# Optimization experiments

Hardware: AMD Instinct MI355X
Metric: run time of the kernel (lower is better)

Reference implementation:

```python
import jax, jax.numpy as jnp
from jax import lax
import numpy as np


def _conv(x, w):
    # x: [B,Cin,H,W], w: [Cout,Cin,kh,kw] -> [B,Cout,H,W], SAME padding
    return lax.conv_general_dilated(x, w, (1, 1), 'SAME')


def setup_inputs() -> dict:
    key = jax.random.key(0)
    ks = jax.random.split(key, 16)
    B, Hh, W = 8, 256, 256
    inputs = jax.random.normal(ks[0], (B, Hh, W), jnp.float32)
    H0 = jax.random.normal(ks[1], (B, Hh, W), jnp.float32)
    C0 = jax.random.normal(ks[2], (B, 2, Hh, W), jnp.float32)
    # learned scalars: c2 ~ U(0,1), sf ~ N(0, 0.01) shifted away from 0 (it is a divisor)
    c2 = jax.random.uniform(ks[3], (1,), jnp.float32, 0.0, 1.0)
    sf = 0.01 * jax.random.normal(ks[4], (1,), jnp.float32) + 0.02
    # RedNet (assumed small conv encoder-decoder): 1->32->64->32->1, 3x3 SAME, ReLU
    w1 = 0.1 * jax.random.normal(ks[5], (32, 1, 3, 3), jnp.float32)
    b1 = jnp.zeros((32,), jnp.float32)
    w2 = 0.1 * jax.random.normal(ks[6], (64, 32, 3, 3), jnp.float32)
    b2 = jnp.zeros((64,), jnp.float32)
    w3 = 0.1 * jax.random.normal(ks[7], (32, 64, 3, 3), jnp.float32)
    b3 = jnp.zeros((32,), jnp.float32)
    w4 = 0.1 * jax.random.normal(ks[8], (1, 32, 3, 3), jnp.float32)
    b4 = jnp.zeros((1,), jnp.float32)
    return dict(inputs=inputs, H0=H0, C0=C0, c2=c2, sf=sf,
                w1=w1, b1=b1, w2=w2, b2=b2, w3=w3, b3=b3, w4=w4, b4=b4)


def reference(inputs, H0, C0, c2, sf, w1, b1, w2, b2, w3, b3, w4, b4):
    # Fixed 5-point Laplacian stencil (non-trainable in the original module)
    lap_k = jnp.array([[0., 1., 0.], [1., -4., 1.], [0., 1., 0.]],
                      dtype=inputs.dtype)[None, None]  # [1,1,3,3]

    # torch chain: C' = permute/matmul(Wcc^T)/permute + wcu*U
    #   reduces exactly to: C'[:,0] = inputs, C'[:,1] = C_old[:,0]
    C_new = jnp.stack([inputs, C0[:, 0]], axis=1)  # [B,2,H,W]

    V = inputs - H0  # [B,H,W]

    # H = whc . C' = 2*C'[:,0] - C'[:,1] = 2*inputs - C_old[:,0]
    lap = _conv(inputs[:, None], lap_k)[:, 0]  # [B,H,W]
    H = 2.0 * inputs - C0[:, 0] + c2 * lap

    # RedNet on scaled residual V
    h = (V / sf)[:, None]  # [B,1,H,W]
    h = jax.nn.relu(_conv(h, w1) + b1[None, :, None, None])
    h = jax.nn.relu(_conv(h, w2) + b2[None, :, None, None])
    h = jax.nn.relu(_conv(h, w3) + b3[None, :, None, None])
    V_hat = (_conv(h, w4) + b4[None, :, None, None])[:, 0] * sf  # [B,H,W]

    outputs = H + V_hat
    return (outputs, H, C_new, V, V_hat)
```

## Files before the change

kernel.cpp:

```cpp
#include <hip/hip_runtime.h>

#define PLANE 65536
#define WIDTH 256
#define PADW 258
#define PADPLANE 66564

typedef __bf16 v8bf __attribute__((ext_vector_type(8)));
typedef float  v4f  __attribute__((ext_vector_type(4)));

typedef const __attribute__((address_space(1))) unsigned int* gas_ptr;
typedef __attribute__((address_space(3))) unsigned int* las_ptr;

__device__ __forceinline__ void gl_lds(const void* g, void* l) {
  __builtin_amdgcn_global_load_lds((gas_ptr)g, (las_ptr)l, 16, 0, 0);
}

__device__ __forceinline__ int swz(int c) {
  return (c & ~7) | ((c & 7) ^ ((c >> 3) & 7));
}

__device__ __forceinline__ unsigned int pack2(float a, float b) {
  __bf16 ba = (__bf16)a, bb = (__bf16)b;
  unsigned short sa = __builtin_bit_cast(unsigned short, ba);
  unsigned short sb = __builtin_bit_cast(unsigned short, bb);
  return (unsigned int)sa | ((unsigned int)sb << 16);
}

__global__ __launch_bounds__(256) void prep_k(
    const float* __restrict__ inputs, const float* __restrict__ H0,
    const float* __restrict__ C0, const float* __restrict__ c2p,
    const float* __restrict__ sfp, float* __restrict__ dout,
    float* __restrict__ vs)
{
  int p = blockIdx.x * 256 + threadIdx.x;
  int b = p >> 16;
  int i = p & 65535;
  int y = i >> 8;
  int x = i & 255;
  float in   = inputs[p];
  float h0   = H0[p];
  float c0a  = C0[b * 131072 + i];
  float up    = (y > 0)   ? inputs[p - 256] : 0.f;
  float down  = (y < 255) ? inputs[p + 256] : 0.f;
  float left  = (x > 0)   ? inputs[p - 1]   : 0.f;
  float right = (x < 255) ? inputs[p + 1]   : 0.f;
  float lap = up + down + left + right - 4.f * in;
  float c2 = c2p[0];
  float sf = sfp[0];
  float Hv = 2.f * in - c0a + c2 * lap;
  float V  = in - h0;
  dout[524288 + p]  = Hv;
  dout[2097152 + p] = V;
  dout[1048576 + b * 131072 + i]         = in;
  dout[1048576 + b * 131072 + 65536 + i] = c0a;
  vs[p] = V / sf;
}

__global__ __launch_bounds__(256) void wtrans_k(
    const float* __restrict__ w1, const float* __restrict__ w2,
    const float* __restrict__ w3, const float* __restrict__ w4,
    float* __restrict__ w1t, __bf16* __restrict__ B2t,
    __bf16* __restrict__ B3t, float* __restrict__ w4t)
{
  int t = blockIdx.x * 256 + threadIdx.x;
  if (t < 288) {
    int tap = t >> 5, cout = t & 31;
    w1t[t] = w1[cout * 9 + tap];
  }
  int t2 = t - 288;
  if (t2 >= 0 && t2 < 18432) {
    int cout = t2 / 288, k = t2 % 288;
    int tap = k / 32, cin = k % 32;
    B2t[t2] = (__bf16)w2[cout * 288 + cin * 9 + tap];
  }
  int t3 = t - (288 + 18432);
  if (t3 >= 0 && t3 < 18432) {
    int cout = t3 / 576, k = t3 % 576;
    int tap = k / 64, cin = k % 64;
    B3t[t3] = (__bf16)w3[cout * 576 + cin * 9 + tap];
  }
  int t4 = t - (288 + 18432 + 18432);
  if (t4 >= 0 && t4 < 288) {
    int tap = t4 >> 5, cin = t4 & 31;
    w4t[t4] = w4[cin * 9 + tap];
  }
}

#define R1 (8 * 1028 * 16)
#define R2 (8 * 1028 * 32)
#define R3 (8 * 1028 * 16)
__global__ __launch_bounds__(256) void zero_k(
    __bf16* __restrict__ a1, __bf16* __restrict__ a2, __bf16* __restrict__ a3)
{
  int t = blockIdx.x * 256 + threadIdx.x;
  unsigned int* p; int C2, idx;
  if (t < R1)            { p = (unsigned int*)a1; C2 = 16; idx = t; }
  else if (t < R1 + R2)  { p = (unsigned int*)a2; C2 = 32; idx = t - R1; }
  else if (t < R1+R2+R3) { p = (unsigned int*)a3; C2 = 16; idx = t - R1 - R2; }
  else return;
  int ch = idx % C2;
  int pr = idx / C2;
  int b = pr / 1028, r = pr % 1028;
  int y, x;
  if      (r < 258) { y = 0;           x = r; }
  else if (r < 516) { y = 257;         x = r - 258; }
  else if (r < 772) { y = r - 516 + 1; x = 0; }
  else              { y = r - 772 + 1; x = 257; }
  p[((size_t)b * PADPLANE + y * PADW + x) * C2 + ch] = 0;
}

__global__ __launch_bounds__(256) void conv1_k(
    const float* __restrict__ vs, const float* __restrict__ w1t,
    const float* __restrict__ b1, __bf16* __restrict__ act1)
{
  int x = threadIdx.x, y = blockIdx.x, b = blockIdx.y;
  const float* ip = vs + ((size_t)b << 16) + y * WIDTH + x;
  float acc[32];
  #pragma unroll
  for (int i = 0; i < 32; i++) acc[i] = b1[i];
  #pragma unroll
  for (int tap = 0; tap < 9; tap++) {
    int dy = tap / 3 - 1, dx = tap % 3 - 1;
    int yy = y + dy, xx = x + dx;
    bool ok = (yy >= 0 && yy < 256 && xx >= 0 && xx < 256);
    float v = ok ? ip[dy * WIDTH + dx] : 0.f;
    const float* wp = w1t + tap * 32;
    #pragma unroll
    for (int i = 0; i < 32; i++) acc[i] = fmaf(wp[i], v, acc[i]);
  }
  unsigned int u[16];
  #pragma unroll
  for (int j = 0; j < 16; j++)
    u[j] = pack2(fmaxf(acc[2*j], 0.f), fmaxf(acc[2*j+1], 0.f));
  size_t pa = ((size_t)b * PADPLANE + (y+1) * PADW + (x+1)) * 32;
  uint4* op = reinterpret_cast<uint4*>(act1 + pa);
  #pragma unroll
  for (int j = 0; j < 4; j++)
    op[j] = make_uint4(u[4*j], u[4*j+1], u[4*j+2], u[4*j+3]);
}

template<int CIN, int COUT, int ROWS>
__global__ __launch_bounds__(256) void conv_lds_k(
    const __bf16* __restrict__ in, const __bf16* __restrict__ Bt,
    const float* __restrict__ bias, __bf16* __restrict__ out)
{
  constexpr int CP    = CIN / 8;
  constexpr int KB    = CIN / 32;
  constexpr int NT    = COUT / 32;
  constexpr int ROWCH = 130 * CP;
  constexpr int ROWB  = ROWCH * 16;
  constexpr int K9    = 9 * CIN;
  constexpr int PWCH  = ROWCH / 4;

  const int lane = threadIdx.x & 63, wave = threadIdx.x >> 6;
  const int l15 = lane & 15, q = lane >> 4;
  const int mw = wave >> 1, nw = wave & 1;
  const int y0 = blockIdx.x * ROWS, xt = blockIdx.y, b = blockIdx.z;
  __shared__ __align__(16) char smem[3 * ROWB];
  const __bf16* plane = in + (size_t)b * PADPLANE * CIN;

  auto stage = [&](int pr, char* lrow) {
    const char* g = (const char*)(plane + ((size_t)pr * PADW + xt * 128) * CIN);
    const int base = wave * PWCH;
    #pragma unroll
    for (int j = 0; j < PWCH / 64; j++) {
      int c = base + j * 64 + lane;
      gl_lds(g + (size_t)swz(c) * 16, lrow + (base + j * 64) * 16);
    }
    if (lane < (PWCH % 64)) {
      int c = base + (PWCH / 64) * 64 + lane;
      gl_lds(g + (size_t)swz(c) * 16, lrow + (base + (PWCH / 64) * 64) * 16);
    }
  };

  v8bf breg[9][KB * NT];
  #pragma unroll
  for (int tap = 0; tap < 9; tap++)
    #pragma unroll
    for (int kb = 0; kb < KB; kb++)
      #pragma unroll
      for (int nt = 0; nt < NT; nt++)
        breg[tap][kb * NT + nt] = *(const v8bf*)(Bt
            + (size_t)(nw * (COUT / 2) + nt * 16 + l15) * K9
            + tap * CIN + kb * 32 + q * 8);

  #pragma unroll
  for (int r = 0; r < 3; r++) stage(y0 + r, smem + r * ROWB);
  __syncthreads();

  for (int i = 0; i < ROWS; i++) {
    v4f acc[4][NT];
    #pragma unroll
    for (int nt = 0; nt < NT; nt++) {
      float bv = bias[nw * (COUT / 2) + nt * 16 + l15];
      #pragma unroll
      for (int mt = 0; mt < 4; mt++) acc[mt][nt] = (v4f){bv, bv, bv, bv};
    }
    #pragma unroll
    for (int tap = 0; tap < 9; tap++) {
      const int dy = tap / 3, dx = tap % 3;
      const char* srow = smem + ((i + dy) % 3) * ROWB;
      #pragma unroll
      for (int kb = 0; kb < KB; kb++) {
        v8bf af[4];
        #pragma unroll
        for (int mt = 0; mt < 4; mt++) {
          int p = mw * 64 + mt * 16 + l15 + dx;
          int G = p * CP + kb * 4 + q;
          af[mt] = *(const v8bf*)(srow + (size_t)swz(G) * 16);
        }
        #pragma unroll
        for (int mt = 0; mt < 4; mt++)
          #pragma unroll
          for (int nt = 0; nt < NT; nt++)
            acc[mt][nt] = __builtin_amdgcn_mfma_f32_16x16x32_bf16(
                af[mt], breg[tap][kb * NT + nt], acc[mt][nt], 0, 0, 0);
      }
    }
    {
      size_t rb = ((size_t)b * PADPLANE + (size_t)(y0 + i + 1) * PADW
                   + xt * 128 + 1) * COUT;
      #pragma unroll
      for (int mt = 0; mt < 4; mt++) {
        #pragma unroll
        for (int r = 0; r < 4; r++) {
          size_t pa = rb + (size_t)(mw * 64 + mt * 16 + q * 4 + r) * COUT;
          #pragma unroll
          for (int nt = 0; nt < NT; nt++)
            out[pa + nw * (COUT / 2) + nt * 16 + l15] =
                (__bf16)fmaxf(acc[mt][nt][r], 0.f);
        }
      }
    }
    __syncthreads();
    if (i + 3 < ROWS + 2)
      stage(y0 + i + 3, smem + (i % 3) * ROWB);
    __syncthreads();
  }
}

#define C4ROWS 4
__global__ __launch_bounds__(256) void conv4_k(
    const __bf16* __restrict__ act3, const float* __restrict__ w4t,
    const float* __restrict__ b4, const float* __restrict__ sfp,
    float* __restrict__ dout)
{
  const int x = threadIdx.x, y0 = blockIdx.x * C4ROWS, b = blockIdx.y;
  const float b4v = b4[0], sf = sfp[0];
  const uint4* base = (const uint4*)(act3 + (size_t)b * PADPLANE * 32);
  float accs[3] = {b4v, b4v, b4v};

  #pragma unroll
  for (int t = 0; t < C4ROWS + 2; t++) {
    const int pr = y0 + t;
    const uint4* rp = base + ((size_t)pr * PADW + x) * 4;
    uint4 L[12];
    #pragma unroll
    for (int j = 0; j < 12; j++) L[j] = rp[j];
    #pragma unroll
    for (int j = 0; j < 12; j++) {
      const int dx = j >> 2, c0 = (j & 3) * 8;
      unsigned int uu[4] = {L[j].x, L[j].y, L[j].z, L[j].w};
      float f[8];
      #pragma unroll
      for (int k = 0; k < 4; k++) {
        f[2*k]   = __builtin_bit_cast(float, uu[k] << 16);
        f[2*k+1] = __builtin_bit_cast(float, uu[k] & 0xFFFF0000u);
      }
      #pragma unroll
      for (int dyp = 0; dyp < 3; dyp++) {
        if (dyp <= t && t - dyp < C4ROWS) {
          const int slot = (t - dyp) % 3;
          const float* wp = w4t + (dyp * 3 + dx) * 32 + c0;
          #pragma unroll
          for (int k = 0; k < 8; k++)
            accs[slot] = fmaf(wp[k], f[k], accs[slot]);
        }
      }
    }
    if (t >= 2) {
      const int r = y0 + t - 2, slot = (t - 2) % 3;
      size_t p0 = ((size_t)b << 16) + (size_t)r * WIDTH + x;
      float vh = accs[slot] * sf;
      dout[p0]           = dout[524288 + p0] + vh;
      dout[2621440 + p0] = vh;
      accs[slot] = b4v;
    }
  }
}

extern "C" void kernel_launch(void* const* d_in, const int* in_sizes, int n_in,
                              void* d_out, int out_size, void* d_ws, size_t ws_size,
                              hipStream_t stream) {
  const float* inputs = (const float*)d_in[0];
  const float* H0     = (const float*)d_in[1];
  const float* C0     = (const float*)d_in[2];
  const float* c2     = (const float*)d_in[3];
  const float* sf     = (const float*)d_in[4];
  const float* w1     = (const float*)d_in[5];
  const float* b1     = (const float*)d_in[6];
  const float* w2     = (const float*)d_in[7];
  const float* b2     = (const float*)d_in[8];
  const float* w3     = (const float*)d_in[9];
  const float* b3     = (const float*)d_in[10];
  const float* w4     = (const float*)d_in[11];
  const float* b4     = (const float*)d_in[12];
  float* out = (float*)d_out;
  float* ws  = (float*)d_ws;

  float*  vs   = ws;
  float*  w1t  = ws + 524288;
  float*  w4t  = ws + 524576;
  __bf16* B2t  = (__bf16*)(ws + 524864);
  __bf16* B3t  = (__bf16*)(ws + 534080);
  __bf16* act1 = (__bf16*)(ws + 543296);
  __bf16* act2 = act1 + (size_t)8 * PADPLANE * 32;
  __bf16* act3 = act2 + (size_t)8 * PADPLANE * 64;

  prep_k<<<2048, 256, 0, stream>>>(inputs, H0, C0, c2, sf, out, vs);
  wtrans_k<<<147, 256, 0, stream>>>(w1, w2, w3, w4, w1t, B2t, B3t, w4t);
  zero_k<<<2056, 256, 0, stream>>>(act1, act2, act3);
  conv1_k<<<dim3(256, 8), 256, 0, stream>>>(vs, w1t, b1, act1);
  conv_lds_k<32, 64, 4><<<dim3(64, 2, 8), 256, 0, stream>>>(act1, B2t, b2, act2);
  conv_lds_k<64, 32, 4><<<dim3(64, 2, 8), 256, 0, stream>>>(act2, B3t, b3, act3);
  conv4_k<<<dim3(64, 8), 256, 0, stream>>>(act3, w4t, b4, sf, out);
}
```

Measured before the change: 192.1 us.

## Specialize conv2/conv3 kernels with full-N waves and two-row reuse in conv3

Replaces the generic templated MFMA conv kernel with two specialized versions. Each wave now covers all output channels for 32 pixels instead of splitting N across waves. conv3 computes two output rows per step from a 4-row LDS ring, so each A fragment loaded from LDS feeds both rows. Both kernels also process 8 rows per block with launch bounds asking for 2 blocks per CU. The aim is fewer LDS reads and less halo restaging per output, at the cost of more registers, larger LDS use and half as many blocks.

```diff
diff --git a/kernel.cpp b/kernel.cpp
--- a/kernel.cpp
+++ b/kernel.cpp
@@ -139,102 +139,196 @@
     op[j] = make_uint4(u[4*j], u[4*j+1], u[4*j+2], u[4*j+3]);
 }
 
-template<int CIN, int COUT, int ROWS>
-__global__ __launch_bounds__(256) void conv_lds_k(
+#define C2ROWB 8320
+template<int ROWS>
+__global__ __launch_bounds__(256, 2) void conv2_k(
     const __bf16* __restrict__ in, const __bf16* __restrict__ Bt,
     const float* __restrict__ bias, __bf16* __restrict__ out)
 {
-  constexpr int CP    = CIN / 8;
-  constexpr int KB    = CIN / 32;
-  constexpr int NT    = COUT / 32;
-  constexpr int ROWCH = 130 * CP;
-  constexpr int ROWB  = ROWCH * 16;
-  constexpr int K9    = 9 * CIN;
-  constexpr int PWCH  = ROWCH / 4;
-
   const int lane = threadIdx.x & 63, wave = threadIdx.x >> 6;
   const int l15 = lane & 15, q = lane >> 4;
-  const int mw = wave >> 1, nw = wave & 1;
   const int y0 = blockIdx.x * ROWS, xt = blockIdx.y, b = blockIdx.z;
-  __shared__ __align__(16) char smem[3 * ROWB];
-  const __bf16* plane = in + (size_t)b * PADPLANE * CIN;
+  const int x0 = xt * 128;
+  __shared__ __align__(16) char smem[3 * C2ROWB];
+  const __bf16* plane = in + (size_t)b * PADPLANE * 32;
 
   auto stage = [&](int pr, char* lrow) {
-    const char* g = (const char*)(plane + ((size_t)pr * PADW + xt * 128) * CIN);
-    const int base = wave * PWCH;
-    #pragma unroll
-    for (int j = 0; j < PWCH / 64; j++) {
+    const char* g = (const char*)(plane + ((size_t)pr * PADW + x0) * 32);
+    const int base = wave * 130;
+    #pragma unroll
+    for (int j = 0; j < 2; j++) {
       int c = base + j * 64 + lane;
       gl_lds(g + (size_t)swz(c) * 16, lrow + (base + j * 64) * 16);
     }
-    if (lane < (PWCH % 64)) {
-      int c = base + (PWCH / 64) * 64 + lane;
-      gl_lds(g + (size_t)swz(c) * 16, lrow + (base + (PWCH / 64) * 64) * 16);
+    if (lane < 2) {
+      int c = base + 128 + lane;
+      gl_lds(g + (size_t)swz(c) * 16, lrow + (base + 128) * 16);
     }
   };
 
-  v8bf breg[9][KB * NT];
+  v8bf breg[9][4];
   #pragma unroll
   for (int tap = 0; tap < 9; tap++)
     #pragma unroll
-    for (int kb = 0; kb < KB; kb++)
-      #pragma unroll
-      for (int nt = 0; nt < NT; nt++)
-        breg[tap][kb * NT + nt] = *(const v8bf*)(Bt
-            + (size_t)(nw * (COUT / 2) + nt * 16 + l15) * K9
-            + tap * CIN + kb * 32 + q * 8);
-
-  #pragma unroll
-  for (int r = 0; r < 3; r++) stage(y0 + r, smem + r * ROWB);
+    for (int nt = 0; nt < 4; nt++)
+      breg[tap][nt] = *(const v8bf*)(Bt + (size_t)(nt * 16 + l15) * 288
+                                        + tap * 32 + q * 8);
+  float bv[4];
+  #pragma unroll
+  for (int nt = 0; nt < 4; nt++) bv[nt] = bias[nt * 16 + l15];
+
+  #pragma unroll
+  for (int r = 0; r < 3; r++) stage(y0 + r, smem + r * C2ROWB);
   __syncthreads();
 
   for (int i = 0; i < ROWS; i++) {
-    v4f acc[4][NT];
-    #pragma unroll
-    for (int nt = 0; nt < NT; nt++) {
-      float bv = bias[nw * (COUT / 2) + nt * 16 + l15];
-      #pragma unroll
-      for (int mt = 0; mt < 4; mt++) acc[mt][nt] = (v4f){bv, bv, bv, bv};
-    }
+    v4f acc[2][4];
+    #pragma unroll
+    for (int mt = 0; mt < 2; mt++)
+      #pragma unroll
+      for (int nt = 0; nt < 4; nt++)
+        acc[mt][nt] = (v4f){bv[nt], bv[nt], bv[nt], bv[nt]};
+
     #pragma unroll
     for (int tap = 0; tap < 9; tap++) {
       const int dy = tap / 3, dx = tap % 3;
-      const char* srow = smem + ((i + dy) % 3) * ROWB;
-      #pragma unroll
-      for (int kb = 0; kb < KB; kb++) {
-        v8bf af[4];
+      const char* srow = smem + ((i + dy) % 3) * C2ROWB;
+      v8bf af[2];
+      #pragma unroll
+      for (int mt = 0; mt < 2; mt++) {
+        int P = wave * 32 + mt * 16 + l15 + dx;
+        af[mt] = *(const v8bf*)(srow + (size_t)swz(P * 4 + q) * 16);
+      }
+      #pragma unroll
+      for (int mt = 0; mt < 2; mt++)
         #pragma unroll
-        for (int mt = 0; mt < 4; mt++) {
-          int p = mw * 64 + mt * 16 + l15 + dx;
-          int G = p * CP + kb * 4 + q;
-          af[mt] = *(const v8bf*)(srow + (size_t)swz(G) * 16);
-        }
-        #pragma unroll
-        for (int mt = 0; mt < 4; mt++)
-          #pragma unroll
-          for (int nt = 0; nt < NT; nt++)
-            acc[mt][nt] = __builtin_amdgcn_mfma_f32_16x16x32_bf16(
-                af[mt], breg[tap][kb * NT + nt], acc[mt][nt], 0, 0, 0);
-      }
+        for (int nt = 0; nt < 4; nt++)
+          acc[mt][nt] = __builtin_amdgcn_mfma_f32_16x16x32_bf16(
+              af[mt], breg[tap][nt], acc[mt][nt], 0, 0, 0);
     }
     {
       size_t rb = ((size_t)b * PADPLANE + (size_t)(y0 + i + 1) * PADW
-                   + xt * 128 + 1) * COUT;
-      #pragma unroll
-      for (int mt = 0; mt < 4; mt++) {
+                   + x0 + 1) * 64;
+      #pragma unroll
+      for (int mt = 0; mt < 2; mt++) {
         #pragma unroll
         for (int r = 0; r < 4; r++) {
-          size_t pa = rb + (size_t)(mw * 64 + mt * 16 + q * 4 + r) * COUT;
+          size_t pa = rb + (size_t)(wave * 32 + mt * 16 + q * 4 + r) * 64;
           #pragma unroll
-          for (int nt = 0; nt < NT; nt++)
-            out[pa + nw * (COUT / 2) + nt * 16 + l15] =
-                (__bf16)fmaxf(acc[mt][nt][r], 0.f);
+          for (int nt = 0; nt < 4; nt++)
+            out[pa + nt * 16 + l15] = (__bf16)fmaxf(acc[mt][nt][r], 0.f);
         }
       }
     }
     __syncthreads();
     if (i + 3 < ROWS + 2)
-      stage(y0 + i + 3, smem + (i % 3) * ROWB);
+      stage(y0 + i + 3, smem + (i % 3) * C2ROWB);
+    __syncthreads();
+  }
+}
+
+#define C3ROWB 16640
+template<int ROWS>
+__global__ __launch_bounds__(256, 2) void conv3_k(
+    const __bf16* __restrict__ in, const __bf16* __restrict__ Bt,
+    const float* __restrict__ bias, __bf16* __restrict__ out)
+{
+  const int lane = threadIdx.x & 63, wave = threadIdx.x >> 6;
+  const int l15 = lane & 15, q = lane >> 4;
+  const int y0 = blockIdx.x * ROWS, xt = blockIdx.y, b = blockIdx.z;
+  const int x0 = xt * 128;
+  __shared__ __align__(16) char smem[4 * C3ROWB];
+  const __bf16* plane = in + (size_t)b * PADPLANE * 64;
+
+  auto stage = [&](int pr, char* lrow) {
+    const char* g = (const char*)(plane + ((size_t)pr * PADW + x0) * 64);
+    const int base = wave * 260;
+    #pragma unroll
+    for (int j = 0; j < 4; j++) {
+      int c = base + j * 64 + lane;
+      gl_lds(g + (size_t)swz(c) * 16, lrow + (base + j * 64) * 16);
+    }
+    if (lane < 4) {
+      int c = base + 256 + lane;
+      gl_lds(g + (size_t)swz(c) * 16, lrow + (base + 256) * 16);
+    }
+  };
+
+  v8bf breg[9][2][2];
+  #pragma unroll
+  for (int tap = 0; tap < 9; tap++)
+    #pragma unroll
+    for (int kb = 0; kb < 2; kb++)
+      #pragma unroll
+      for (int nt = 0; nt < 2; nt++)
+        breg[tap][kb][nt] = *(const v8bf*)(Bt + (size_t)(nt * 16 + l15) * 576
+                                              + tap * 64 + kb * 32 + q * 8);
+  float bv[2] = {bias[l15], bias[16 + l15]};
+
+  #pragma unroll
+  for (int r = 0; r < 4; r++) stage(y0 + r, smem + r * C3ROWB);
+  __syncthreads();
+
+  for (int ps = 0; ps < ROWS / 2; ps++) {
+    v4f acc[2][2][2];
+    #pragma unroll
+    for (int rr = 0; rr < 2; rr++)
+      #pragma unroll
+      for (int mt = 0; mt < 2; mt++)
+        #pragma unroll
+        for (int nt = 0; nt < 2; nt++)
+          acc[rr][mt][nt] = (v4f){bv[nt], bv[nt], bv[nt], bv[nt]};
+
+    #pragma unroll
+    for (int t = 0; t < 4; t++) {
+      const char* srow = smem + ((2 * ps + t) & 3) * C3ROWB;
+      #pragma unroll
+      for (int dx = 0; dx < 3; dx++) {
+        #pragma unroll
+        for (int kb = 0; kb < 2; kb++) {
+          v8bf af[2];
+          #pragma unroll
+          for (int mt = 0; mt < 2; mt++) {
+            int P = wave * 32 + mt * 16 + l15 + dx;
+            af[mt] = *(const v8bf*)(srow + (size_t)swz(P * 8 + kb * 4 + q) * 16);
+          }
+          #pragma unroll
+          for (int mt = 0; mt < 2; mt++)
+            #pragma unroll
+            for (int nt = 0; nt < 2; nt++) {
+              if (t <= 2)
+                acc[0][mt][nt] = __builtin_amdgcn_mfma_f32_16x16x32_bf16(
+                    af[mt], breg[t * 3 + dx][kb][nt], acc[0][mt][nt], 0, 0, 0);
+              if (t >= 1)
+                acc[1][mt][nt] = __builtin_amdgcn_mfma_f32_16x16x32_bf16(
+                    af[mt], breg[(t - 1) * 3 + dx][kb][nt], acc[1][mt][nt],
+                    0, 0, 0);
+            }
+        }
+      }
+    }
+    {
+      #pragma unroll
+      for (int rr = 0; rr < 2; rr++) {
+        size_t rb = ((size_t)b * PADPLANE
+                     + (size_t)(y0 + 2 * ps + rr + 1) * PADW + x0 + 1) * 32;
+        #pragma unroll
+        for (int mt = 0; mt < 2; mt++) {
+          #pragma unroll
+          for (int r = 0; r < 4; r++) {
+            size_t pa = rb + (size_t)(wave * 32 + mt * 16 + q * 4 + r) * 32;
+            #pragma unroll
+            for (int nt = 0; nt < 2; nt++)
+              out[pa + nt * 16 + l15] = (__bf16)fmaxf(acc[rr][mt][nt][r], 0.f);
+          }
+        }
+      }
+    }
+    __syncthreads();
+    if (ps + 1 < ROWS / 2) {
+      stage(y0 + 2 * ps + 4, smem + ((2 * ps) & 3) * C3ROWB);
+      stage(y0 + 2 * ps + 5, smem + ((2 * ps + 1) & 3) * C3ROWB);
+    }
     __syncthreads();
   }
 }
@@ -321,7 +415,7 @@
   wtrans_k<<<147, 256, 0, stream>>>(w1, w2, w3, w4, w1t, B2t, B3t, w4t);
   zero_k<<<2056, 256, 0, stream>>>(act1, act2, act3);
   conv1_k<<<dim3(256, 8), 256, 0, stream>>>(vs, w1t, b1, act1);
-  conv_lds_k<32, 64, 4><<<dim3(64, 2, 8), 256, 0, stream>>>(act1, B2t, b2, act2);
-  conv_lds_k<64, 32, 4><<<dim3(64, 2, 8), 256, 0, stream>>>(act2, B3t, b3, act3);
+  conv2_k<8><<<dim3(32, 2, 8), 256, 0, stream>>>(act1, B2t, b2, act2);
+  conv3_k<8><<<dim3(32, 2, 8), 256, 0, stream>>>(act2, B3t, b3, act3);
   conv4_k<<<dim3(64, 8), 256, 0, stream>>>(act3, w4t, b4, sf, out);
 }
```

Result: faster. 187.8 us (-2.3%).

## Fuse conv2 and conv3 into one kernel keeping act2 rows in LDS

Applied to the files above, without the earlier changes.

Replaces the two separate conv_lds_k launches with a single conv23_k that computes conv2 rows into a rolling 3-row LDS buffer and immediately consumes them for conv3, so the 64-channel act2 tensor is never written to or read from global memory. The act2 padding zeroing is dropped from zero_k accordingly. Tiles become 32-row by 64-column slabs, with halo recomputation at the column edges and a grid of only 256 blocks with launch_bounds(256,1). This cuts global traffic at the cost of lower parallelism, halo recompute, and more syncs per row.

```diff
diff --git a/kernel.cpp b/kernel.cpp
--- a/kernel.cpp
+++ b/kernel.cpp
@@ -87,26 +87,24 @@
 }
 
 #define R1 (8 * 1028 * 16)
-#define R2 (8 * 1028 * 32)
 #define R3 (8 * 1028 * 16)
 __global__ __launch_bounds__(256) void zero_k(
-    __bf16* __restrict__ a1, __bf16* __restrict__ a2, __bf16* __restrict__ a3)
+    __bf16* __restrict__ a1, __bf16* __restrict__ a3)
 {
   int t = blockIdx.x * 256 + threadIdx.x;
-  unsigned int* p; int C2, idx;
-  if (t < R1)            { p = (unsigned int*)a1; C2 = 16; idx = t; }
-  else if (t < R1 + R2)  { p = (unsigned int*)a2; C2 = 32; idx = t - R1; }
-  else if (t < R1+R2+R3) { p = (unsigned int*)a3; C2 = 16; idx = t - R1 - R2; }
+  unsigned int* p; int idx;
+  if (t < R1)            { p = (unsigned int*)a1; idx = t; }
+  else if (t < R1 + R3)  { p = (unsigned int*)a3; idx = t - R1; }
   else return;
-  int ch = idx % C2;
-  int pr = idx / C2;
+  int ch = idx & 15;
+  int pr = idx >> 4;
   int b = pr / 1028, r = pr % 1028;
   int y, x;
   if      (r < 258) { y = 0;           x = r; }
   else if (r < 516) { y = 257;         x = r - 258; }
   else if (r < 772) { y = r - 516 + 1; x = 0; }
   else              { y = r - 772 + 1; x = 257; }
-  p[((size_t)b * PADPLANE + y * PADW + x) * C2 + ch] = 0;
+  p[((size_t)b * PADPLANE + y * PADW + x) * 16 + ch] = 0;
 }
 
 __global__ __launch_bounds__(256) void conv1_k(
@@ -139,102 +137,167 @@
     op[j] = make_uint4(u[4*j], u[4*j+1], u[4*j+2], u[4*j+3]);
 }
 
-template<int CIN, int COUT, int ROWS>
-__global__ __launch_bounds__(256) void conv_lds_k(
-    const __bf16* __restrict__ in, const __bf16* __restrict__ Bt,
-    const float* __restrict__ bias, __bf16* __restrict__ out)
-{
-  constexpr int CP    = CIN / 8;
-  constexpr int KB    = CIN / 32;
-  constexpr int NT    = COUT / 32;
-  constexpr int ROWCH = 130 * CP;
-  constexpr int ROWB  = ROWCH * 16;
-  constexpr int K9    = 9 * CIN;
-  constexpr int PWCH  = ROWCH / 4;
+#define A1SLOT 5376
+#define A2SLOT 10496
+#define SLAB23 32
+
+__global__ __launch_bounds__(256, 1) void conv23_k(
+    const __bf16* __restrict__ act1, const __bf16* __restrict__ B2t,
+    const __bf16* __restrict__ B3t, const float* __restrict__ b2,
+    const float* __restrict__ b3, __bf16* __restrict__ act3)
+{
+  __shared__ __align__(16) char sm1[4 * A1SLOT];
+  __shared__ __align__(16) char sm2[3 * A2SLOT];
 
   const int lane = threadIdx.x & 63, wave = threadIdx.x >> 6;
   const int l15 = lane & 15, q = lane >> 4;
-  const int mw = wave >> 1, nw = wave & 1;
-  const int y0 = blockIdx.x * ROWS, xt = blockIdx.y, b = blockIdx.z;
-  __shared__ __align__(16) char smem[3 * ROWB];
-  const __bf16* plane = in + (size_t)b * PADPLANE * CIN;
-
-  auto stage = [&](int pr, char* lrow) {
-    const char* g = (const char*)(plane + ((size_t)pr * PADW + xt * 128) * CIN);
-    const int base = wave * PWCH;
-    #pragma unroll
-    for (int j = 0; j < PWCH / 64; j++) {
-      int c = base + j * 64 + lane;
-      gl_lds(g + (size_t)swz(c) * 16, lrow + (base + j * 64) * 16);
-    }
-    if (lane < (PWCH % 64)) {
-      int c = base + (PWCH / 64) * 64 + lane;
-      gl_lds(g + (size_t)swz(c) * 16, lrow + (base + (PWCH / 64) * 64) * 16);
+  const int y0 = blockIdx.x * SLAB23;
+  const int x0 = blockIdx.y * 64;
+  const int b  = blockIdx.z;
+  const int s2 = (x0 == 0) ? 1 : 0;
+  const int z2 = (x0 == 0) ? 0 : ((x0 == 192) ? 65 : -1);
+  const int gcol0 = x0 - 1;
+  const int nmt = (wave == 0) ? 2 : 1;
+
+  const char* plane1 = (const char*)(act1 + (size_t)b * PADPLANE * 32);
+
+  v8bf b2r[9][4];
+  float bv2[4];
+  #pragma unroll
+  for (int tap = 0; tap < 9; tap++)
+    #pragma unroll
+    for (int nt = 0; nt < 4; nt++)
+      b2r[tap][nt] = *(const v8bf*)(B2t + (size_t)(nt * 16 + l15) * 288
+                                        + tap * 32 + q * 8);
+  #pragma unroll
+  for (int nt = 0; nt < 4; nt++) bv2[nt] = b2[nt * 16 + l15];
+
+  v8bf b3r[9][2][2];
+  float bv3[2];
+  #pragma unroll
+  for (int tap = 0; tap < 9; tap++)
+    #pragma unroll
+    for (int kb = 0; kb < 2; kb++)
+      #pragma unroll
+      for (int nt = 0; nt < 2; nt++)
+        b3r[tap][kb][nt] = *(const v8bf*)(B3t + (size_t)(nt * 16 + l15) * 576
+                                              + tap * 64 + kb * 32 + q * 8);
+  bv3[0] = b3[l15]; bv3[1] = b3[16 + l15];
+
+  auto stage1 = [&](int rr) {
+    if (rr < -1 || rr > 256) return;
+    char* lrow = sm1 + (size_t)((rr + 4) & 3) * A1SLOT;
+    const char* g = plane1 + (long)((rr + 1) * PADW + gcol0) * 64;
+    const int base = wave * 68;
+    {
+      int c = base + lane;
+      gl_lds(g + (long)swz(c) * 16, lrow + (size_t)base * 16);
+    }
+    if (lane < 4) {
+      int c = base + 64 + lane;
+      gl_lds(g + (long)swz(c) * 16, lrow + (size_t)(base + 64) * 16);
     }
   };
 
-  v8bf breg[9][KB * NT];
-  #pragma unroll
-  for (int tap = 0; tap < 9; tap++)
-    #pragma unroll
-    for (int kb = 0; kb < KB; kb++)
-      #pragma unroll
-      for (int nt = 0; nt < NT; nt++)
-        breg[tap][kb * NT + nt] = *(const v8bf*)(Bt
-            + (size_t)(nw * (COUT / 2) + nt * 16 + l15) * K9
-            + tap * CIN + kb * 32 + q * 8);
-
-  #pragma unroll
-  for (int r = 0; r < 3; r++) stage(y0 + r, smem + r * ROWB);
-  __syncthreads();
-
-  for (int i = 0; i < ROWS; i++) {
-    v4f acc[4][NT];
-    #pragma unroll
-    for (int nt = 0; nt < NT; nt++) {
-      float bv = bias[nw * (COUT / 2) + nt * 16 + l15];
-      #pragma unroll
-      for (int mt = 0; mt < 4; mt++) acc[mt][nt] = (v4f){bv, bv, bv, bv};
-    }
+  auto conv2row = [&](int n2) {
+    char* wr = sm2 + (size_t)(((n2 % 3) + 3) % 3) * A2SLOT;
+    if (n2 < 0 || n2 > 255) {
+      for (int c = threadIdx.x; c < 528; c += 256)
+        *(uint4*)(wr + (size_t)c * 16) = make_uint4(0, 0, 0, 0);
+      return;
+    }
+    const char* a1p[3];
+    #pragma unroll
+    for (int dy = 0; dy < 3; dy++)
+      a1p[dy] = sm1 + (size_t)((n2 - 1 + dy + 4) & 3) * A1SLOT;
+    v4f acc[2][4];
+    #pragma unroll
+    for (int mi = 0; mi < 2; mi++)
+      #pragma unroll
+      for (int nt = 0; nt < 4; nt++)
+        acc[mi][nt] = (v4f){bv2[nt], bv2[nt], bv2[nt], bv2[nt]};
     #pragma unroll
     for (int tap = 0; tap < 9; tap++) {
       const int dy = tap / 3, dx = tap % 3;
-      const char* srow = smem + ((i + dy) % 3) * ROWB;
-      #pragma unroll
-      for (int kb = 0; kb < KB; kb++) {
-        v8bf af[4];
+      v8bf af[2];
+      #pragma unroll
+      for (int mi = 0; mi < 2; mi++) if (mi < nmt) {
+        int tile = (mi == 0) ? wave : 4;
+        int w = s2 + tile * 16 + l15 + dx;
+        af[mi] = *(const v8bf*)(a1p[dy] + (size_t)swz(w * 4 + q) * 16);
+      }
+      #pragma unroll
+      for (int mi = 0; mi < 2; mi++) if (mi < nmt)
         #pragma unroll
-        for (int mt = 0; mt < 4; mt++) {
-          int p = mw * 64 + mt * 16 + l15 + dx;
-          int G = p * CP + kb * 4 + q;
-          af[mt] = *(const v8bf*)(srow + (size_t)swz(G) * 16);
-        }
+        for (int nt = 0; nt < 4; nt++)
+          acc[mi][nt] = __builtin_amdgcn_mfma_f32_16x16x32_bf16(
+              af[mi], b2r[tap][nt], acc[mi][nt], 0, 0, 0);
+    }
+    #pragma unroll
+    for (int mi = 0; mi < 2; mi++) if (mi < nmt) {
+      int tile = (mi == 0) ? wave : 4;
+      #pragma unroll
+      for (int r = 0; r < 4; r++) {
+        int p = s2 + tile * 16 + q * 4 + r;
         #pragma unroll
-        for (int mt = 0; mt < 4; mt++)
-          #pragma unroll
-          for (int nt = 0; nt < NT; nt++)
-            acc[mt][nt] = __builtin_amdgcn_mfma_f32_16x16x32_bf16(
-                af[mt], breg[tap][kb * NT + nt], acc[mt][nt], 0, 0, 0);
-      }
-    }
-    {
-      size_t rb = ((size_t)b * PADPLANE + (size_t)(y0 + i + 1) * PADW
-                   + xt * 128 + 1) * COUT;
-      #pragma unroll
-      for (int mt = 0; mt < 4; mt++) {
-        #pragma unroll
-        for (int r = 0; r < 4; r++) {
-          size_t pa = rb + (size_t)(mw * 64 + mt * 16 + q * 4 + r) * COUT;
-          #pragma unroll
-          for (int nt = 0; nt < NT; nt++)
-            out[pa + nw * (COUT / 2) + nt * 16 + l15] =
-                (__bf16)fmaxf(acc[mt][nt][r], 0.f);
+        for (int nt = 0; nt < 4; nt++) {
+          int c = p * 8 + nt * 2 + (l15 >> 3);
+          *(__bf16*)(wr + (size_t)swz(c) * 16 + (l15 & 7) * 2) =
+              (__bf16)fmaxf(acc[mi][nt][r], 0.f);
         }
       }
     }
+    if (z2 >= 0 && threadIdx.x < 8)
+      *(uint4*)(wr + (size_t)swz(z2 * 8 + (int)threadIdx.x) * 16) =
+          make_uint4(0, 0, 0, 0);
+  };
+
+  auto conv3row = [&](int r3) {
+    v4f acc[2];
+    #pragma unroll
+    for (int nt = 0; nt < 2; nt++)
+      acc[nt] = (v4f){bv3[nt], bv3[nt], bv3[nt], bv3[nt]};
+    #pragma unroll
+    for (int t = 0; t < 3; t++) {
+      const char* ar = sm2 + (size_t)((r3 - 1 + t + 3) % 3) * A2SLOT;
+      #pragma unroll
+      for (int dx = 0; dx < 3; dx++)
+        #pragma unroll
+        for (int kb = 0; kb < 2; kb++) {
+          int j = wave * 16 + l15;
+          v8bf af = *(const v8bf*)(ar
+              + (size_t)swz((j + dx) * 8 + kb * 4 + q) * 16);
+          #pragma unroll
+          for (int nt = 0; nt < 2; nt++)
+            acc[nt] = __builtin_amdgcn_mfma_f32_16x16x32_bf16(
+                af, b3r[t * 3 + dx][kb][nt], acc[nt], 0, 0, 0);
+        }
+    }
+    size_t rb = ((size_t)b * PADPLANE + (size_t)(r3 + 1) * PADW + x0 + 1) * 32;
+    #pragma unroll
+    for (int r = 0; r < 4; r++) {
+      int j = wave * 16 + q * 4 + r;
+      #pragma unroll
+      for (int nt = 0; nt < 2; nt++)
+        act3[rb + (size_t)j * 32 + nt * 16 + l15] =
+            (__bf16)fmaxf(acc[nt][r], 0.f);
+    }
+  };
+
+  stage1(y0 - 2); stage1(y0 - 1); stage1(y0); stage1(y0 + 1);
+  __syncthreads();
+  conv2row(y0 - 1);
+  __syncthreads();
+  stage1(y0 + 2);
+  conv2row(y0);
+  __syncthreads();
+
+  for (int i = 0; i < SLAB23; i++) {
+    int r = y0 + i;
+    stage1(r + 3);
+    conv2row(r + 1);
     __syncthreads();
-    if (i + 3 < ROWS + 2)
-      stage(y0 + i + 3, smem + (i % 3) * ROWB);
+    conv3row(r);
     __syncthreads();
   }
 }
@@ -314,14 +377,13 @@
   __bf16* B2t  = (__bf16*)(ws + 524864);
   __bf16* B3t  = (__bf16*)(ws + 534080);
   __bf16* act1 = (__bf16*)(ws + 543296);
-  __bf16* act2 = act1 + (size_t)8 * PADPLANE * 32;
-  __bf16* act3 = act2 + (size_t)8 * PADPLANE * 64;
+  __bf16* act3 = act1 + (size_t)8 * PADPLANE * 32
+                      + (size_t)8 * PADPLANE * 64;
 
   prep_k<<<2048, 256, 0, stream>>>(inputs, H0, C0, c2, sf, out, vs);
   wtrans_k<<<147, 256, 0, stream>>>(w1, w2, w3, w4, w1t, B2t, B3t, w4t);
-  zero_k<<<2056, 256, 0, stream>>>(act1, act2, act3);
+  zero_k<<<1028, 256, 0, stream>>>(act1, act3);
   conv1_k<<<dim3(256, 8), 256, 0, stream>>>(vs, w1t, b1, act1);
-  conv_lds_k<32, 64, 4><<<dim3(64, 2, 8), 256, 0, stream>>>(act1, B2t, b2, act2);
-  conv_lds_k<64, 32, 4><<<dim3(64, 2, 8), 256, 0, stream>>>(act2, B3t, b3, act3);
+  conv23_k<<<dim3(8, 4, 8), 256, 0, stream>>>(act1, B2t, B3t, b2, b3, act3);
   conv4_k<<<dim3(64, 8), 256, 0, stream>>>(act3, w4t, b4, sf, out);
 }
```

After: 249.1 us. 29.6% more time.
